# Optimization experiments

Hardware: AMD Instinct MI355X
Metric: run time of the kernel (lower is better)

Reference implementation:

```python
import jax, jax.numpy as jnp
import numpy as np

UNITS = 400
FEAT = 3
B, T = 128, 1000


def setup_inputs() -> dict:
    key = jax.random.key(0)
    ks = jax.random.split(key, 8)
    s = 0.08  # small init scale
    return {
        "x": jax.random.normal(ks[0], (B, T, FEAT), dtype=jnp.float32),
        "W": jax.random.normal(ks[1], (FEAT, 4 * UNITS), dtype=jnp.float32) * s,
        "U": jax.random.normal(ks[2], (UNITS, 4 * UNITS), dtype=jnp.float32) * s,
        "b": jnp.zeros((4 * UNITS,), dtype=jnp.float32),
        "p_i": jax.random.normal(ks[3], (UNITS,), dtype=jnp.float32) * s,
        "p_f": jax.random.normal(ks[4], (UNITS,), dtype=jnp.float32) * s,
        "p_o": jax.random.normal(ks[5], (UNITS,), dtype=jnp.float32) * s,
        "Wd": jax.random.normal(ks[6], (UNITS, FEAT), dtype=jnp.float32) * s,
        "bd": jnp.zeros((FEAT,), dtype=jnp.float32),
    }


def reference(x, W, U, b, p_i, p_f, p_o, Wd, bd):
    """Peephole LSTM (Graves) scan + dense projection.

    Gate order i, f, g(cell candidate), o. Peepholes: i,f see c_{t-1}; o sees c_t.
    """
    batch = x.shape[0]
    units = U.shape[0]
    # Precompute input contribution for all timesteps: [B, T, 4U]
    xw = jnp.einsum("btf,fg->btg", x, W) + b

    def step(carry, xw_t):
        h, c = carry  # [B, U] each
        z = xw_t + h @ U  # [B, 4U]
        zi, zf, zg, zo = jnp.split(z, 4, axis=-1)
        i = jax.nn.sigmoid(zi + p_i * c)
        f = jax.nn.sigmoid(zf + p_f * c)
        c_new = f * c + i * jnp.tanh(zg)
        o = jax.nn.sigmoid(zo + p_o * c_new)
        h_new = o * jnp.tanh(c_new)
        return (h_new, c_new), h_new

    init = (jnp.zeros((batch, units), x.dtype), jnp.zeros((batch, units), x.dtype))
    _, hs = jax.lax.scan(step, init, jnp.swapaxes(xw, 0, 1))  # hs: [T, B, U]
    hs = jnp.swapaxes(hs, 0, 1)  # [B, T, U]
    return hs @ Wd + bd  # [B, T, FEAT]
```

## Files before the change

### kernel.cpp

```cpp
#include <hip/hip_runtime.h>
#include <hip/hip_bf16.h>

#define UNITS   400
#define BATCH   128
#define TSTEPS  1000
#define GATES   1600
#define KCAP    448
#define NGROUP  8
#define CWG     20
#define SU      20
#define UW      4
#define NW      5
#define NTHR    320
#define ROWS    16
#define OUTSZ   (BATCH*TSTEPS*3)
#define NSLICE  5
#define SPIN_GUARD 16384

typedef __bf16 bf16x8 __attribute__((ext_vector_type(8)));
typedef float  f32x4  __attribute__((ext_vector_type(4)));
typedef unsigned long long ull;

__device__ __forceinline__ float sigm(float v)     { return 1.f / (1.f + __expf(-v)); }
__device__ __forceinline__ float tanhfast(float v) { return 1.f - 2.f / (1.f + __expf(2.f * v)); }

__device__ __forceinline__ unsigned short f2bf(float v) {
    __hip_bfloat16 h = __float2bfloat16(v);
    return *reinterpret_cast<unsigned short*>(&h);
}

__global__ void hw_init_kernel(const float* __restrict__ U, const float* __restrict__ W,
                               const float* __restrict__ b,
                               unsigned short* __restrict__ Urep, float* __restrict__ Wrep,
                               float* __restrict__ brep, unsigned short* __restrict__ Hbuf,
                               int* __restrict__ flags, float* __restrict__ outP)
{
    int idx = blockIdx.x * 256 + threadIdx.x;
    if (idx < GATES * KCAP) {
        int col = idx / KCAP, k = idx - col * KCAP;
        int u = col >> 2, G = col & 3;
        float v = (k < UNITS) ? U[k * GATES + G * UNITS + u] : 0.f;
        Urep[idx] = f2bf(v);
        return;
    }
    idx -= GATES * KCAP;
    if (idx < 3 * GATES) {
        int f = idx / GATES, col = idx - f * GATES;
        int u = col >> 2, G = col & 3;
        Wrep[idx] = W[f * GATES + G * UNITS + u];
        return;
    }
    idx -= 3 * GATES;
    if (idx < GATES) {
        int u = idx >> 2, G = idx & 3;
        brep[idx] = b[G * UNITS + u];
        return;
    }
    idx -= GATES;
    if (idx < 2 * BATCH * KCAP) { Hbuf[idx] = 0; return; }
    idx -= 2 * BATCH * KCAP;
    if (idx < NGROUP * 128) { flags[idx] = 0; return; }
    idx -= NGROUP * 128;
    if (idx < NSLICE * OUTSZ) { outP[idx] = 0.f; return; }
}

#define LDA(i, offlit) \
    asm volatile("global_load_dwordx4 %0, %1, off offset:" offlit " sc0 sc1" \
                 : "=v"(af[i]) : "v"(ab) : "memory");

__global__ __launch_bounds__(NTHR, 1) void lstm_kernel(
    const float* __restrict__ x,
    const float* __restrict__ p_i, const float* __restrict__ p_f, const float* __restrict__ p_o,
    const float* __restrict__ Wd,
    const unsigned short* __restrict__ Urep,
    const float* __restrict__ Wrep, const float* __restrict__ brep,
    unsigned short* __restrict__ Hbuf,
    int* __restrict__ flags,
    float* __restrict__ outP)
{
    __shared__ float redw[NW * ROWS * 3];

    const int tid  = threadIdx.x;
    const int lane = tid & 63, wid = tid >> 6;
    const int bid  = blockIdx.x;
    const int grp  = bid & 7;
    const int c    = bid >> 3;
    const int b0   = grp * ROWS;
    const int uw   = c * SU + wid * UW;
    const int col0 = uw * 4;
    const int row  = lane & 15;
    const int kg   = lane >> 4;
    const int gu   = uw + kg;

    bf16x8 barr[13];
    {
        const unsigned short* up = Urep + (size_t)(col0 + row) * KCAP + kg * 8;
        #pragma unroll
        for (int kt = 0; kt < 13; ++kt)
            barr[kt] = *(const bf16x8*)(up + kt * 32);
    }

    float w0[4], w1[4], w2[4], bz[4];
    #pragma unroll
    for (int G = 0; G < 4; ++G) {
        w0[G] = Wrep[0 * GATES + gu * 4 + G];
        w1[G] = Wrep[1 * GATES + gu * 4 + G];
        w2[G] = Wrep[2 * GATES + gu * 4 + G];
        bz[G] = brep[gu * 4 + G];
    }
    const float pi = p_i[gu], pf = p_f[gu], po = p_o[gu];
    const float wd0 = Wd[gu * 3 + 0], wd1 = Wd[gu * 3 + 1], wd2 = Wd[gu * 3 + 2];

    const size_t bufbytes = (size_t)BATCH * KCAP * 2;
    const char* arb0 = (const char*)Hbuf + ((size_t)(b0 + row) * KCAP + kg * 8) * 2;
    const char* arb1 = arb0 + bufbytes;
    char* awb0 = (char*)Hbuf + ((size_t)(b0 + lane) * KCAP + uw) * 2;
    char* awb1 = awb0 + bufbytes;

    int* fl    = flags + grp * 128;
    int* slotp = fl + c;
    const int pidx = (lane < CWG) ? lane : 0;
    const float* xp = x + (size_t)(b0 + row) * (TSTEPS * 3);
    float* opp = outP + (size_t)(c % NSLICE) * OUTSZ + (size_t)b0 * (TSTEPS * 3);

    const int S  = ((lane & 12) << 2) + (kg << 2);
    const int jj = lane & 3;
    float cst = 0.f;

    #pragma unroll 1
    for (int t = 0; t < TSTEPS; ++t) {
        float x0 = xp[t * 3 + 0], x1 = xp[t * 3 + 1], x2 = xp[t * 3 + 2];

        {
            int guard = 0;
            for (;;) {
                int f = __hip_atomic_load(fl + pidx, __ATOMIC_RELAXED, __HIP_MEMORY_SCOPE_AGENT);
                if (__all(f >= t)) break;
                if (++guard >= SPIN_GUARD) break;
                __builtin_amdgcn_s_sleep(1);
            }
        }

        f32x4 af[13];
        const char* ab = (t & 1) ? arb1 : arb0;
        LDA(0, "0")   LDA(1, "64")  LDA(2, "128") LDA(3, "192")
        LDA(4, "256") LDA(5, "320") LDA(6, "384") LDA(7, "448")
        LDA(8, "512") LDA(9, "576") LDA(10, "640") LDA(11, "704") LDA(12, "768")
        asm volatile("s_waitcnt vmcnt(0)" ::: "memory");
        __builtin_amdgcn_sched_barrier(0);

        f32x4 a0 = {0.f, 0.f, 0.f, 0.f}, a1 = {0.f, 0.f, 0.f, 0.f};
        #pragma unroll
        for (int kt = 0; kt < 13; kt += 2)
            a0 = __builtin_amdgcn_mfma_f32_16x16x32_bf16(
                     __builtin_bit_cast(bf16x8, af[kt]), barr[kt], a0, 0, 0, 0);
        #pragma unroll
        for (int kt = 1; kt < 13; kt += 2)
            a1 = __builtin_amdgcn_mfma_f32_16x16x32_bf16(
                     __builtin_bit_cast(bf16x8, af[kt]), barr[kt], a1, 0, 0, 0);
        f32x4 acc = a0 + a1;

        float zz[4];
        {
            float q0[4], q1[4], q2[4], q3[4];
            #pragma unroll
            for (int G = 0; G < 4; ++G) {
                q0[G] = __shfl(acc[0], S + G);
                q1[G] = __shfl(acc[1], S + G);
                q2[G] = __shfl(acc[2], S + G);
                q3[G] = __shfl(acc[3], S + G);
            }
            #pragma unroll
            for (int G = 0; G < 4; ++G) {
                float r = q0[G];
                r = (jj == 1) ? q1[G] : r;
                r = (jj == 2) ? q2[G] : r;
                r = (jj == 3) ? q3[G] : r;
                zz[G] = r + bz[G] + x0 * w0[G] + x1 * w1[G] + x2 * w2[G];
            }
        }

        float iv = sigm(zz[0] + pi * cst);
        float fv = sigm(zz[1] + pf * cst);
        float cn = fv * cst + iv * tanhfast(zz[2]);
        float ov = sigm(zz[3] + po * cn);
        float h  = ov * tanhfast(cn);
        cst = cn;

        int hb = (int)f2bf(h);
        int h1 = __shfl_down(hb, 16);
        int h2 = __shfl_down(hb, 32);
        int h3 = __shfl_down(hb, 48);
        if (lane < 16) {
            unsigned int lo = (unsigned int)(hb & 0xffff) | ((unsigned int)(h1 & 0xffff) << 16);
            unsigned int hi = (unsigned int)(h2 & 0xffff) | ((unsigned int)(h3 & 0xffff) << 16);
            ull pk = (ull)lo | ((ull)hi << 32);
            ull* dst = (ull*)((t & 1) ? awb0 : awb1);
            __hip_atomic_store(dst, pk, __ATOMIC_RELAXED, __HIP_MEMORY_SCOPE_AGENT);
        }

        float s0 = h * wd0, s1 = h * wd1, s2 = h * wd2;
        s0 += __shfl_xor(s0, 16); s0 += __shfl_xor(s0, 32);
        s1 += __shfl_xor(s1, 16); s1 += __shfl_xor(s1, 32);
        s2 += __shfl_xor(s2, 16); s2 += __shfl_xor(s2, 32);
        if (lane < 16) {
            redw[wid * (ROWS * 3) + lane * 3 + 0] = s0;
            redw[wid * (ROWS * 3) + lane * 3 + 1] = s1;
            redw[wid * (ROWS * 3) + lane * 3 + 2] = s2;
        }

        asm volatile("s_waitcnt vmcnt(0)" ::: "memory");
        __syncthreads();

        if (tid == 0)
            __hip_atomic_store(slotp, t + 1, __ATOMIC_RELAXED, __HIP_MEMORY_SCOPE_AGENT);

        if (tid < 48) {
            int r = tid & 15, f = tid >> 4;
            float s = 0.f;
            #pragma unroll
            for (int w2 = 0; w2 < NW; ++w2) s += redw[w2 * (ROWS * 3) + r * 3 + f];
            atomicAdd(opp + (size_t)r * (TSTEPS * 3) + t * 3 + f, s);
        }
    }
}

__global__ void merge_kernel(const float* __restrict__ outP, const float* __restrict__ bd,
                             float* __restrict__ out)
{
    int i = blockIdx.x * 256 + threadIdx.x;
    if (i >= OUTSZ) return;
    float s = bd[i % 3];
    #pragma unroll
    for (int k = 0; k < NSLICE; ++k) s += outP[(size_t)k * OUTSZ + i];
    out[i] = s;
}

extern "C" void kernel_launch(void* const* d_in, const int* in_sizes, int n_in,
                              void* d_out, int out_size, void* d_ws, size_t ws_size,
                              hipStream_t stream)
{
    const float* x   = (const float*)d_in[0];
    const float* W   = (const float*)d_in[1];
    const float* U   = (const float*)d_in[2];
    const float* b   = (const float*)d_in[3];
    const float* p_i = (const float*)d_in[4];
    const float* p_f = (const float*)d_in[5];
    const float* p_o = (const float*)d_in[6];
    const float* Wd  = (const float*)d_in[7];
    const float* bd  = (const float*)d_in[8];
    float* out = (float*)d_out;

    char* p = (char*)d_ws;
    unsigned short* Urep = (unsigned short*)p;  p += (size_t)GATES * KCAP * 2;
    float* Wrep = (float*)p;                    p += (size_t)3 * GATES * 4;
    float* brep = (float*)p;                    p += (size_t)GATES * 4;
    unsigned short* Hbuf = (unsigned short*)p;  p += (size_t)2 * BATCH * KCAP * 2;
    int* flags = (int*)p;                       p += (size_t)NGROUP * 128 * 4;
    float* outP = (float*)p;                    p += (size_t)NSLICE * OUTSZ * 4;

    const int total = GATES * KCAP + 3 * GATES + GATES + 2 * BATCH * KCAP
                    + NGROUP * 128 + NSLICE * OUTSZ;
    const int iblocks = (total + 255) / 256;
    hipLaunchKernelGGL(hw_init_kernel, dim3(iblocks), dim3(256), 0, stream,
                       U, W, b, Urep, Wrep, brep, Hbuf, flags, outP);

    hipLaunchKernelGGL(lstm_kernel, dim3(NGROUP * CWG), dim3(NTHR), 0, stream,
                       x, p_i, p_f, p_o, Wd, Urep, Wrep, brep, Hbuf, flags, outP);

    hipLaunchKernelGGL(merge_kernel, dim3((OUTSZ + 255) / 256), dim3(256), 0, stream,
                       outP, bd, out);
}
```

Before: 3.718 ms.

## Embed step epochs in hidden-state stores and split K across waves

Removes the separate per-block flag array. Each 16-byte hidden-state store now carries the timestep counter next to the data, so consumers poll the data itself and can use it once the tags match. This takes the store-wait, the flag store and the flag-then-data round trip out of the critical path. Work is also repartitioned: each wave handles a K-slice across all 5 column tiles, and the partial sums are reduced through shared memory with an extra barrier per step. The cost is twice the hidden-state memory traffic, because of the tags, plus an LDS reduction.

```diff
diff --git a/kernel.cpp b/kernel.cpp
--- a/kernel.cpp
+++ b/kernel.cpp
@@ -5,45 +5,51 @@
 #define BATCH   128
 #define TSTEPS  1000
 #define GATES   1600
-#define KCAP    448
+#define KCAP2   480
+#define NKT     15
 #define NGROUP  8
 #define CWG     20
 #define SU      20
-#define UW      4
 #define NW      5
 #define NTHR    320
 #define ROWS    16
+#define SLOTS   120
+#define RSLOTS  100
+#define ROWB    (SLOTS*16)
+#define GRPB    (ROWS*ROWB)
+#define PARB    (NGROUP*GRPB)
 #define OUTSZ   (BATCH*TSTEPS*3)
 #define NSLICE  5
 #define SPIN_GUARD 16384
 
 typedef __bf16 bf16x8 __attribute__((ext_vector_type(8)));
 typedef float  f32x4  __attribute__((ext_vector_type(4)));
-typedef unsigned long long ull;
+typedef unsigned int u32x4 __attribute__((ext_vector_type(4)));
 
 __device__ __forceinline__ float sigm(float v)     { return 1.f / (1.f + __expf(-v)); }
 __device__ __forceinline__ float tanhfast(float v) { return 1.f - 2.f / (1.f + __expf(2.f * v)); }
 
-__device__ __forceinline__ unsigned short f2bf(float v) {
+__device__ __forceinline__ unsigned int f2bf(float v) {
     __hip_bfloat16 h = __float2bfloat16(v);
-    return *reinterpret_cast<unsigned short*>(&h);
+    return (unsigned int)*reinterpret_cast<unsigned short*>(&h);
 }
 
 __global__ void hw_init_kernel(const float* __restrict__ U, const float* __restrict__ W,
                                const float* __restrict__ b,
                                unsigned short* __restrict__ Urep, float* __restrict__ Wrep,
-                               float* __restrict__ brep, unsigned short* __restrict__ Hbuf,
-                               int* __restrict__ flags, float* __restrict__ outP)
+                               float* __restrict__ brep, int* __restrict__ Hep,
+                               float* __restrict__ outP)
 {
     int idx = blockIdx.x * 256 + threadIdx.x;
-    if (idx < GATES * KCAP) {
-        int col = idx / KCAP, k = idx - col * KCAP;
+    if (idx < GATES * KCAP2) {
+        int col = idx / KCAP2, k = idx - col * KCAP2;
         int u = col >> 2, G = col & 3;
         float v = (k < UNITS) ? U[k * GATES + G * UNITS + u] : 0.f;
-        Urep[idx] = f2bf(v);
+        __hip_bfloat16 h = __float2bfloat16(v);
+        Urep[idx] = *reinterpret_cast<unsigned short*>(&h);
         return;
     }
-    idx -= GATES * KCAP;
+    idx -= GATES * KCAP2;
     if (idx < 3 * GATES) {
         int f = idx / GATES, col = idx - f * GATES;
         int u = col >> 2, G = col & 3;
@@ -57,16 +63,10 @@
         return;
     }
     idx -= GATES;
-    if (idx < 2 * BATCH * KCAP) { Hbuf[idx] = 0; return; }
-    idx -= 2 * BATCH * KCAP;
-    if (idx < NGROUP * 128) { flags[idx] = 0; return; }
-    idx -= NGROUP * 128;
+    if (idx < 2 * PARB / 4) { Hep[idx] = 0; return; }
+    idx -= 2 * PARB / 4;
     if (idx < NSLICE * OUTSZ) { outP[idx] = 0.f; return; }
 }
-
-#define LDA(i, offlit) \
-    asm volatile("global_load_dwordx4 %0, %1, off offset:" offlit " sc0 sc1" \
-                 : "=v"(af[i]) : "v"(ab) : "memory");
 
 __global__ __launch_bounds__(NTHR, 1) void lstm_kernel(
     const float* __restrict__ x,
@@ -74,10 +74,10 @@
     const float* __restrict__ Wd,
     const unsigned short* __restrict__ Urep,
     const float* __restrict__ Wrep, const float* __restrict__ brep,
-    unsigned short* __restrict__ Hbuf,
-    int* __restrict__ flags,
+    char* __restrict__ Hep,
     float* __restrict__ outP)
 {
+    __shared__ float zpart[NW * 5 * 64 * 4];
     __shared__ float redw[NW * ROWS * 3];
 
     const int tid  = threadIdx.x;
@@ -86,20 +86,31 @@
     const int grp  = bid & 7;
     const int c    = bid >> 3;
     const int b0   = grp * ROWS;
-    const int uw   = c * SU + wid * UW;
-    const int col0 = uw * 4;
+    const int col0 = c * SU * 4;
     const int row  = lane & 15;
     const int kg   = lane >> 4;
-    const int gu   = uw + kg;
-
-    bf16x8 barr[13];
-    {
-        const unsigned short* up = Urep + (size_t)(col0 + row) * KCAP + kg * 8;
+
+    bf16x8 barr[5][3];
+    #pragma unroll
+    for (int n = 0; n < 5; ++n) {
+        const unsigned short* up =
+            Urep + (size_t)(col0 + n * 16 + row) * KCAP2 + (wid * 3) * 32 + kg * 8;
         #pragma unroll
-        for (int kt = 0; kt < 13; ++kt)
-            barr[kt] = *(const bf16x8*)(up + kt * 32);
-    }
-
+        for (int kk = 0; kk < 3; ++kk)
+            barr[n][kk] = *(const bf16x8*)(up + kk * 32);
+    }
+
+    bool rv[3][2];
+    #pragma unroll
+    for (int kk = 0; kk < 3; ++kk) {
+        int s = 8 * (wid * 3 + kk) + 2 * kg;
+        rv[kk][0] = (s     < RSLOTS);
+        rv[kk][1] = (s + 1 < RSLOTS);
+    }
+
+    const int pr = tid & 15;
+    const int pu = tid >> 4;
+    const int gu = c * SU + pu;
     float w0[4], w1[4], w2[4], bz[4];
     #pragma unroll
     for (int G = 0; G < 4; ++G) {
@@ -111,75 +122,84 @@
     const float pi = p_i[gu], pf = p_f[gu], po = p_o[gu];
     const float wd0 = Wd[gu * 3 + 0], wd1 = Wd[gu * 3 + 1], wd2 = Wd[gu * 3 + 2];
 
-    const size_t bufbytes = (size_t)BATCH * KCAP * 2;
-    const char* arb0 = (const char*)Hbuf + ((size_t)(b0 + row) * KCAP + kg * 8) * 2;
-    const char* arb1 = arb0 + bufbytes;
-    char* awb0 = (char*)Hbuf + ((size_t)(b0 + lane) * KCAP + uw) * 2;
-    char* awb1 = awb0 + bufbytes;
-
-    int* fl    = flags + grp * 128;
-    int* slotp = fl + c;
-    const int pidx = (lane < CWG) ? lane : 0;
-    const float* xp = x + (size_t)(b0 + row) * (TSTEPS * 3);
+    const char* ldb0 = Hep + grp * GRPB + (size_t)row * ROWB + wid * 384 + kg * 32;
+    const char* ldb1 = ldb0 + PARB;
+    char* stb0 = Hep + grp * GRPB + (size_t)lane * ROWB + (c * 5 + wid) * 16;
+    char* stb1 = stb0 + PARB;
+
+    const float* xp = x + (size_t)(b0 + pr) * (TSTEPS * 3);
     float* opp = outP + (size_t)(c % NSLICE) * OUTSZ + (size_t)b0 * (TSTEPS * 3);
 
-    const int S  = ((lane & 12) << 2) + (kg << 2);
-    const int jj = lane & 3;
     float cst = 0.f;
 
     #pragma unroll 1
     for (int t = 0; t < TSTEPS; ++t) {
         float x0 = xp[t * 3 + 0], x1 = xp[t * 3 + 1], x2 = xp[t * 3 + 2];
 
+        u32x4 sa0, sb0, sa1, sb1, sa2, sb2;
         {
+            const char* ab = (t & 1) ? ldb1 : ldb0;
+            const unsigned int te = (unsigned int)t;
             int guard = 0;
             for (;;) {
-                int f = __hip_atomic_load(fl + pidx, __ATOMIC_RELAXED, __HIP_MEMORY_SCOPE_AGENT);
-                if (__all(f >= t)) break;
+                asm volatile("global_load_dwordx4 %0, %1, off sc0 sc1"
+                             : "=v"(sa0) : "v"(ab) : "memory");
+                asm volatile("global_load_dwordx4 %0, %1, off offset:16 sc0 sc1"
+                             : "=v"(sb0) : "v"(ab) : "memory");
+                asm volatile("global_load_dwordx4 %0, %1, off offset:128 sc0 sc1"
+                             : "=v"(sa1) : "v"(ab) : "memory");
+                asm volatile("global_load_dwordx4 %0, %1, off offset:144 sc0 sc1"
+                             : "=v"(sb1) : "v"(ab) : "memory");
+                asm volatile("global_load_dwordx4 %0, %1, off offset:256 sc0 sc1"
+                             : "=v"(sa2) : "v"(ab) : "memory");
+                asm volatile("global_load_dwordx4 %0, %1, off offset:272 sc0 sc1"
+                             : "=v"(sb2) : "v"(ab) : "memory");
+                asm volatile("s_waitcnt vmcnt(0)" ::: "memory");
+                bool ok = (!rv[0][0] || (sa0[1] == te && sa0[3] == te))
+                       && (!rv[0][1] || (sb0[1] == te && sb0[3] == te))
+                       && (!rv[1][0] || (sa1[1] == te && sa1[3] == te))
+                       && (!rv[1][1] || (sb1[1] == te && sb1[3] == te))
+                       && (!rv[2][0] || (sa2[1] == te && sa2[3] == te))
+                       && (!rv[2][1] || (sb2[1] == te && sb2[3] == te));
+                if (__all((int)ok)) break;
                 if (++guard >= SPIN_GUARD) break;
                 __builtin_amdgcn_s_sleep(1);
             }
         }
 
-        f32x4 af[13];
-        const char* ab = (t & 1) ? arb1 : arb0;
-        LDA(0, "0")   LDA(1, "64")  LDA(2, "128") LDA(3, "192")
-        LDA(4, "256") LDA(5, "320") LDA(6, "384") LDA(7, "448")
-        LDA(8, "512") LDA(9, "576") LDA(10, "640") LDA(11, "704") LDA(12, "768")
-        asm volatile("s_waitcnt vmcnt(0)" ::: "memory");
-        __builtin_amdgcn_sched_barrier(0);
-
-        f32x4 a0 = {0.f, 0.f, 0.f, 0.f}, a1 = {0.f, 0.f, 0.f, 0.f};
+        f32x4 acc[5] = {};
+        {
+            u32x4 f0 = {sa0[0], sa0[2], sb0[0], sb0[2]};
+            u32x4 f1 = {sa1[0], sa1[2], sb1[0], sb1[2]};
+            u32x4 f2 = {sa2[0], sa2[2], sb2[0], sb2[2]};
+            bf16x8 a0 = __builtin_bit_cast(bf16x8, f0);
+            bf16x8 a1 = __builtin_bit_cast(bf16x8, f1);
+            bf16x8 a2 = __builtin_bit_cast(bf16x8, f2);
+            #pragma unroll
+            for (int n = 0; n < 5; ++n) {
+                acc[n] = __builtin_amdgcn_mfma_f32_16x16x32_bf16(a0, barr[n][0], acc[n], 0, 0, 0);
+                acc[n] = __builtin_amdgcn_mfma_f32_16x16x32_bf16(a1, barr[n][1], acc[n], 0, 0, 0);
+                acc[n] = __builtin_amdgcn_mfma_f32_16x16x32_bf16(a2, barr[n][2], acc[n], 0, 0, 0);
+            }
+        }
         #pragma unroll
-        for (int kt = 0; kt < 13; kt += 2)
-            a0 = __builtin_amdgcn_mfma_f32_16x16x32_bf16(
-                     __builtin_bit_cast(bf16x8, af[kt]), barr[kt], a0, 0, 0, 0);
+        for (int n = 0; n < 5; ++n)
+            *(f32x4*)&zpart[(((wid * 5) + n) * 64 + lane) * 4] = acc[n];
+        __syncthreads();
+
+        float zz[4];
         #pragma unroll
-        for (int kt = 1; kt < 13; kt += 2)
-            a1 = __builtin_amdgcn_mfma_f32_16x16x32_bf16(
-                     __builtin_bit_cast(bf16x8, af[kt]), barr[kt], a1, 0, 0, 0);
-        f32x4 acc = a0 + a1;
-
-        float zz[4];
-        {
-            float q0[4], q1[4], q2[4], q3[4];
+        for (int G = 0; G < 4; ++G) {
+            int cc = pu * 4 + G;
+            int n  = cc >> 4;
+            int ls = ((pr >> 2) << 4) + (cc & 15);
+            int j  = pr & 3;
+            float s = 0.f;
             #pragma unroll
-            for (int G = 0; G < 4; ++G) {
-                q0[G] = __shfl(acc[0], S + G);
-                q1[G] = __shfl(acc[1], S + G);
-                q2[G] = __shfl(acc[2], S + G);
-                q3[G] = __shfl(acc[3], S + G);
-            }
-            #pragma unroll
-            for (int G = 0; G < 4; ++G) {
-                float r = q0[G];
-                r = (jj == 1) ? q1[G] : r;
-                r = (jj == 2) ? q2[G] : r;
-                r = (jj == 3) ? q3[G] : r;
-                zz[G] = r + bz[G] + x0 * w0[G] + x1 * w1[G] + x2 * w2[G];
-            }
-        }
-
+            for (int w = 0; w < NW; ++w)
+                s += zpart[(((w * 5) + n) * 64 + ls) * 4 + j];
+            zz[G] = s + bz[G] + x0 * w0[G] + x1 * w1[G] + x2 * w2[G];
+        }
         float iv = sigm(zz[0] + pi * cst);
         float fv = sigm(zz[1] + pf * cst);
         float cn = fv * cst + iv * tanhfast(zz[2]);
@@ -187,16 +207,17 @@
         float h  = ov * tanhfast(cn);
         cst = cn;
 
-        int hb = (int)f2bf(h);
-        int h1 = __shfl_down(hb, 16);
-        int h2 = __shfl_down(hb, 32);
-        int h3 = __shfl_down(hb, 48);
+        unsigned int hb = f2bf(h);
+        unsigned int h1 = __shfl_down((int)hb, 16);
+        unsigned int h2 = __shfl_down((int)hb, 32);
+        unsigned int h3 = __shfl_down((int)hb, 48);
         if (lane < 16) {
-            unsigned int lo = (unsigned int)(hb & 0xffff) | ((unsigned int)(h1 & 0xffff) << 16);
-            unsigned int hi = (unsigned int)(h2 & 0xffff) | ((unsigned int)(h3 & 0xffff) << 16);
-            ull pk = (ull)lo | ((ull)hi << 32);
-            ull* dst = (ull*)((t & 1) ? awb0 : awb1);
-            __hip_atomic_store(dst, pk, __ATOMIC_RELAXED, __HIP_MEMORY_SCOPE_AGENT);
+            unsigned int lo = (hb & 0xffffu) | (h1 << 16);
+            unsigned int hi = (h2 & 0xffffu) | (h3 << 16);
+            u32x4 sv = {lo, (unsigned int)(t + 1), hi, (unsigned int)(t + 1)};
+            char* dst = (t & 1) ? stb0 : stb1;
+            asm volatile("global_store_dwordx4 %0, %1, off sc0 sc1"
+                         :: "v"(dst), "v"(sv) : "memory");
         }
 
         float s0 = h * wd0, s1 = h * wd1, s2 = h * wd2;
@@ -208,13 +229,7 @@
             redw[wid * (ROWS * 3) + lane * 3 + 1] = s1;
             redw[wid * (ROWS * 3) + lane * 3 + 2] = s2;
         }
-
-        asm volatile("s_waitcnt vmcnt(0)" ::: "memory");
         __syncthreads();
-
-        if (tid == 0)
-            __hip_atomic_store(slotp, t + 1, __ATOMIC_RELAXED, __HIP_MEMORY_SCOPE_AGENT);
-
         if (tid < 48) {
             int r = tid & 15, f = tid >> 4;
             float s = 0.f;
@@ -252,21 +267,19 @@
     float* out = (float*)d_out;
 
     char* p = (char*)d_ws;
-    unsigned short* Urep = (unsigned short*)p;  p += (size_t)GATES * KCAP * 2;
+    unsigned short* Urep = (unsigned short*)p;  p += (size_t)GATES * KCAP2 * 2;
     float* Wrep = (float*)p;                    p += (size_t)3 * GATES * 4;
     float* brep = (float*)p;                    p += (size_t)GATES * 4;
-    unsigned short* Hbuf = (unsigned short*)p;  p += (size_t)2 * BATCH * KCAP * 2;
-    int* flags = (int*)p;                       p += (size_t)NGROUP * 128 * 4;
+    char* Hep = p;                              p += (size_t)2 * PARB;
     float* outP = (float*)p;                    p += (size_t)NSLICE * OUTSZ * 4;
 
-    const int total = GATES * KCAP + 3 * GATES + GATES + 2 * BATCH * KCAP
-                    + NGROUP * 128 + NSLICE * OUTSZ;
+    const int total = GATES * KCAP2 + 3 * GATES + GATES + 2 * PARB / 4 + NSLICE * OUTSZ;
     const int iblocks = (total + 255) / 256;
     hipLaunchKernelGGL(hw_init_kernel, dim3(iblocks), dim3(256), 0, stream,
-                       U, W, b, Urep, Wrep, brep, Hbuf, flags, outP);
+                       U, W, b, Urep, Wrep, brep, (int*)Hep, outP);
 
     hipLaunchKernelGGL(lstm_kernel, dim3(NGROUP * CWG), dim3(NTHR), 0, stream,
-                       x, p_i, p_f, p_o, Wd, Urep, Wrep, brep, Hbuf, flags, outP);
+                       x, p_i, p_f, p_o, Wd, Urep, Wrep, brep, Hep, outP);
 
     hipLaunchKernelGGL(merge_kernel, dim3((OUTSZ + 255) / 256), dim3(256), 0, stream,
                        outP, bd, out);
```

New measurement: 3.668 ms. About the same (-1.4%).
